# Kernel tuning notes

Measured on AMD Instinct MI355X. Metric: run time of the kernel, lower is better.

## Reference

```python
import jax, jax.numpy as jnp
import numpy as np

NV, NC = 4096, 16384        # n_vars, n_clauses
VL, CL = 8, 8               # vlabel_dim (ground_dim), clabel_dim
VE, CE = 128, 128           # vemb_dim, cemb_dim
ITERS = 4                   # max_iters
LN_EPS = 1e-5


def setup_inputs() -> dict:
    key = jax.random.key(0)
    ks = jax.random.split(key, 10)
    return {
        "vlabels": jax.random.normal(ks[0], (NV, VL), jnp.float32),
        "clabels": jax.random.normal(ks[1], (NC, CL), jnp.float32),
        "cmat_pos": jax.random.uniform(ks[2], (NC, NV), jnp.float32),
        "cmat_neg": jax.random.uniform(ks[3], (NC, NV), jnp.float32),
        "W_V_pos": jax.random.normal(ks[4], (VL + VE, CE), jnp.float32),
        "W_V_neg": jax.random.normal(ks[5], (VL + VE, CE), jnp.float32),
        "B_V": jax.random.normal(ks[6], (CE,), jnp.float32),
        "W_C_pos": jax.random.normal(ks[7], (CL + CE, VE), jnp.float32),
        "W_C_neg": jax.random.normal(ks[8], (CL + CE, VE), jnp.float32),
        "B_C": jax.random.normal(ks[9], (VE,), jnp.float32),
        "ln_gamma": jnp.ones((VE,), jnp.float32),
        "ln_beta": jnp.zeros((VE,), jnp.float32),
    }


def _layernorm(x, gamma, beta):
    mu = jnp.mean(x, axis=-1, keepdims=True)
    var = jnp.var(x, axis=-1, keepdims=True)
    return (x - mu) * jax.lax.rsqrt(var + LN_EPS) * gamma + beta


def reference(vlabels, clabels, cmat_pos, cmat_neg,
              W_V_pos, W_V_neg, B_V, W_C_pos, W_C_neg, B_C,
              ln_gamma, ln_beta):
    n_vars = vlabels.shape[0]
    vmat_pos = cmat_pos.T  # [NV, NC]
    vmat_neg = cmat_neg.T
    vembs0 = jnp.zeros((n_vars, VE), vlabels.dtype)

    def step(vembs, _):
        vs = jnp.concatenate([vlabels, vembs], axis=1)          # [NV, VL+VE]
        pv = vs @ W_V_pos                                       # [NV, CE]
        nv = vs @ W_V_neg
        cembs = jax.nn.relu(cmat_pos @ pv + cmat_neg @ nv + B_V)  # [NC, CE]
        cs = jnp.concatenate([clabels, cembs], axis=1)          # [NC, CL+CE]
        pc = cs @ W_C_pos                                       # [NC, VE]
        nc = cs @ W_C_neg
        v = jax.nn.relu(vmat_pos @ pc + vmat_neg @ nc + B_C)    # [NV, VE]
        v = _layernorm(v, ln_gamma, ln_beta)
        return v, None

    vembs, _ = jax.lax.scan(step, vembs0, None, length=ITERS)
    return vembs
```

## Files before the change

kernel.cpp:

```cpp
#include <hip/hip_runtime.h>

#define NVV 4096
#define NCC 16384
#define AS1 __attribute__((address_space(1)))
#define AS3 __attribute__((address_space(3)))

typedef __attribute__((ext_vector_type(8))) short short8;
typedef __attribute__((ext_vector_type(4))) short short4v;
typedef __attribute__((ext_vector_type(4))) float f32x4;

__device__ __forceinline__ short f2bf(float f) {
  union { float f; unsigned u; } v; v.f = f;
  unsigned r = v.u + 0x7fffu + ((v.u >> 16) & 1u);
  return (short)(r >> 16);
}

template<typename AT>
__device__ __forceinline__ short8 load8v(const AT* p) {
  if constexpr (sizeof(AT) == 2) {
    return *(const short8*)p;
  } else {
    const f32x4* q = (const f32x4*)p;
    f32x4 a = q[0], b = q[1];
    short8 o;
#pragma unroll
    for (int j = 0; j < 4; ++j) { o[j] = f2bf(a[j]); o[j + 4] = f2bf(b[j]); }
    return o;
  }
}

__global__ __launch_bounds__(256) void k_conv(const float* __restrict__ src,
                                              short* __restrict__ dst, int n8) {
  int i = blockIdx.x * blockDim.x + threadIdx.x;
  const int stride = gridDim.x * blockDim.x;
  for (; i < n8; i += stride) {
    const f32x4* q = (const f32x4*)(src + (size_t)i * 8);
    f32x4 a = q[0], b = q[1];
    short8 o;
#pragma unroll
    for (int j = 0; j < 4; ++j) { o[j] = f2bf(a[j]); o[j + 4] = f2bf(b[j]); }
    *(short8*)(dst + (size_t)i * 8) = o;
  }
}

__global__ __launch_bounds__(256) void k_convT(const float* __restrict__ src,
                                               short* __restrict__ dstN,
                                               short* __restrict__ dstT,
                                               int R, int C) {
  __shared__ short t[64][66];
  const int r0 = blockIdx.y * 64, c0 = blockIdx.x * 64;
  const int tr = threadIdx.x >> 2;
  const int q  = (threadIdx.x & 3) << 4;
  const float* s = src + (size_t)(r0 + tr) * C + c0 + q;
  const f32x4 v0 = *(const f32x4*)(s);
  const f32x4 v1 = *(const f32x4*)(s + 4);
  const f32x4 v2 = *(const f32x4*)(s + 8);
  const f32x4 v3 = *(const f32x4*)(s + 12);
  short8 a, b;
#pragma unroll
  for (int j = 0; j < 4; ++j) {
    a[j] = f2bf(v0[j]); a[4 + j] = f2bf(v1[j]);
    b[j] = f2bf(v2[j]); b[4 + j] = f2bf(v3[j]);
  }
  short* dn = dstN + (size_t)(r0 + tr) * C + c0 + q;
  *(short8*)dn = a;
  *(short8*)(dn + 8) = b;
#pragma unroll
  for (int j = 0; j < 8; ++j) { t[tr][q + j] = a[j]; t[tr][q + 8 + j] = b[j]; }
  __syncthreads();
  short8 oa, ob;
#pragma unroll
  for (int j = 0; j < 8; ++j) { oa[j] = t[q + j][tr]; ob[j] = t[q + 8 + j][tr]; }
  short* dt = dstT + (size_t)(c0 + tr) * R + r0 + q;
  *(short8*)dt = oa;
  *(short8*)(dt + 8) = ob;
}

template<int SRC, int NROW>
__global__ __launch_bounds__(128) void k_mlp(
    const float* __restrict__ labels, const float* __restrict__ embs,
    const float* __restrict__ bias,
    const float* __restrict__ Wp, const float* __restrict__ Wn,
    short* __restrict__ Tp, short* __restrict__ Tn, int Nrows, int KS) {
  __shared__ float xs[NROW][129];
  const int n = threadIdx.x;
  const int m0 = blockIdx.x * NROW;
  if (SRC == 1) {
#pragma unroll
    for (int r = 0; r < NROW; ++r)
      xs[r][n] = embs[(size_t)(m0 + r) * 128 + n];
    __syncthreads();
  } else if (SRC == 2) {
#pragma unroll
    for (int r = 0; r < NROW; ++r) {
      const size_t m = m0 + r;
      float v = bias[n];
      for (int ks = 0; ks < KS; ++ks)
        v += embs[((size_t)ks * NCC + m) * 128 + n];
      xs[r][n] = fmaxf(v, 0.f);
    }
    __syncthreads();
  }
  float ap[NROW] = {}, an[NROW] = {};
  const int JMAX = (SRC == 0) ? 8 : 136;
  for (int j = 0; j < JMAX; ++j) {
    const float wp = Wp[j * 128 + n], wn = Wn[j * 128 + n];
#pragma unroll
    for (int r = 0; r < NROW; ++r) {
      float x;
      if (j < 8) x = labels[(size_t)(m0 + r) * 8 + j];
      else       x = xs[r][j - 8];
      ap[r] = fmaf(x, wp, ap[r]);
      an[r] = fmaf(x, wn, an[r]);
    }
  }
  short8 vp0, vn0, vp1, vn1;
#pragma unroll
  for (int r = 0; r < 8; ++r) {
    vp0[r] = f2bf(ap[r]); vn0[r] = f2bf(an[r]);
    vp1[r] = f2bf(ap[8 + r]); vn1[r] = f2bf(an[8 + r]);
  }
  *(short8*)(Tp + (size_t)n * Nrows + m0) = vp0;
  *(short8*)(Tp + (size_t)n * Nrows + m0 + 8) = vp1;
  *(short8*)(Tn + (size_t)n * Nrows + m0) = vn0;
  *(short8*)(Tn + (size_t)n * Nrows + m0 + 8) = vn1;
}

template<int LSK>
__global__ __launch_bounds__(256, 2) void k_gemm8(
    const short* __restrict__ Ap, const short* __restrict__ An,
    const short* __restrict__ Bp, const short* __restrict__ Bn,
    float* __restrict__ C, int M, int lda, int ldb, int Klen) {
  __shared__ __align__(16) short sb[2][16384];
  const int tid = threadIdx.x;
  const int w = tid >> 6, l = tid & 63, lr = l & 15, lh = l >> 4;
  const int wr = w >> 1, wc = w & 1;
  const int id = blockIdx.x;
  const int zw = id & ((1 << LSK) - 1);
  const int m0 = (id >> LSK) * 128;
  const int Koff = zw * Klen;
  const int T = Klen >> 5;

  const int srow = (w << 4) + (l >> 2);
  const int scol = ((l & 3) ^ (srow & 3)) << 3;
  const short* gAp = Ap + (size_t)(m0 + srow) * lda + Koff + scol;
  const short* gAn = An + (size_t)(m0 + srow) * lda + Koff + scol;
  const short* gBp = Bp + (size_t)srow * ldb + Koff + scol;
  const short* gBn = Bn + (size_t)srow * ldb + Koff + scol;

  f32x4 acc[4][4] = {};

  auto stage = [&](int kstep, int buf) {
    const int k0 = kstep << 5;
    short* db = &sb[buf][0];
#pragma unroll
    for (int i = 0; i < 2; ++i) {
      const size_t ra = (size_t)(i * 64) * lda + k0;
      const size_t rb = (size_t)(i * 64) * ldb + k0;
      const int d = (i * 256 + w * 64) * 8;
      __builtin_amdgcn_global_load_lds((const AS1 void*)(gAp + ra),
                                       (AS3 void*)(db + d), 16, 0, 0);
      __builtin_amdgcn_global_load_lds((const AS1 void*)(gAn + ra),
                                       (AS3 void*)(db + 4096 + d), 16, 0, 0);
      __builtin_amdgcn_global_load_lds((const AS1 void*)(gBp + rb),
                                       (AS3 void*)(db + 8192 + d), 16, 0, 0);
      __builtin_amdgcn_global_load_lds((const AS1 void*)(gBn + rb),
                                       (AS3 void*)(db + 12288 + d), 16, 0, 0);
    }
  };

  stage(0, 0);
  asm volatile("s_waitcnt vmcnt(0)" ::: "memory");
  __builtin_amdgcn_s_barrier();
  asm volatile("" ::: "memory");

  for (int t = 0; t < T; ++t) {
    stage((t + 1 < T) ? t + 1 : 0, (t + 1) & 1);
    const short* bp = &sb[t & 1][0];
    short8 a[2][4], b[2][4];
#pragma unroll
    for (int mi = 0; mi < 4; ++mi) {
      const int row = (wr << 6) + (mi << 4) + lr;
      const int ad = (row << 5) + ((lh ^ (row & 3)) << 3);
      a[0][mi] = *(const short8*)&bp[ad];
      a[1][mi] = *(const short8*)&bp[4096 + ad];
    }
#pragma unroll
    for (int nj = 0; nj < 4; ++nj) {
      const int n = (wc << 6) + (nj << 4) + lr;
      const int bd = (n << 5) + ((lh ^ (n & 3)) << 3);
      b[0][nj] = *(const short8*)&bp[8192 + bd];
      b[1][nj] = *(const short8*)&bp[12288 + bd];
    }
#pragma unroll
    for (int mat = 0; mat < 2; ++mat)
#pragma unroll
      for (int mi = 0; mi < 4; ++mi)
#pragma unroll
        for (int nj = 0; nj < 4; ++nj)
          acc[mi][nj] = __builtin_amdgcn_mfma_f32_16x16x32_bf16(
              a[mat][mi], b[mat][nj], acc[mi][nj], 0, 0, 0);
    asm volatile("s_waitcnt vmcnt(0)" ::: "memory");
    __builtin_amdgcn_s_barrier();
    asm volatile("" ::: "memory");
  }

#pragma unroll
  for (int mi = 0; mi < 4; ++mi)
#pragma unroll
    for (int nj = 0; nj < 4; ++nj) {
      const int col = (wc << 6) + (nj << 4) + lr;
#pragma unroll
      for (int r = 0; r < 4; ++r) {
        const int m = m0 + (wr << 6) + (mi << 4) + (lh << 2) + r;
        C[((size_t)zw * M + m) * 128 + col] = acc[mi][nj][r];
      }
    }
}

template<typename AT, bool TRANSA, int EPI>
__global__ __launch_bounds__(256) void k_gemm(
    const AT* __restrict__ Ap, const AT* __restrict__ An,
    const short* __restrict__ Bp, const short* __restrict__ Bn,
    const float* __restrict__ bias, float* __restrict__ C,
    int M, int lda, int ldb, int Klen) {
  __shared__ __align__(16) short sA[2][32 * 64];
  __shared__ __align__(16) short sB[2][64 * 64];
  const int tid = threadIdx.x;
  const int w = tid >> 6, l = tid & 63, lr = l & 15, lh = l >> 4;
  const int m0 = blockIdx.x * 32, n0 = blockIdx.y * 64;
  const int Koff = blockIdx.z * Klen;
  f32x4 acc0 = {0.f, 0.f, 0.f, 0.f}, acc1 = {0.f, 0.f, 0.f, 0.f};

  for (int step = 0; step < (Klen >> 6); ++step) {
    const int k0 = Koff + (step << 6);
    __syncthreads();
    if (!TRANSA) {
      const int m = tid >> 3, kc = tid & 7;
      const size_t ga = (size_t)(m0 + m) * lda + k0 + (kc << 3);
      const int ad = (m << 6) + ((kc ^ (m & 7)) << 3);
      *(short8*)&sA[0][ad] = load8v(Ap + ga);
      *(short8*)&sA[1][ad] = load8v(An + ga);
    } else {
      const int r = tid >> 2, c8 = (tid & 3) << 3;
      const size_t ga = (size_t)(k0 + r) * lda + m0 + c8;
      short8 vp = load8v(Ap + ga), vn = load8v(An + ga);
#pragma unroll
      for (int j = 0; j < 8; ++j) {
        const int m = c8 + j;
        const int ad = (m << 6) + ((((r >> 3)) ^ (m & 7)) << 3) + (r & 7);
        sA[0][ad] = vp[j];
        sA[1][ad] = vn[j];
      }
    }
#pragma unroll
    for (int i = 0; i < 2; ++i) {
      const int c = (i << 8) + tid;
      const int n = c >> 3, kc = c & 7;
      const size_t gb = (size_t)(n0 + n) * ldb + k0 + (kc << 3);
      const int ad = (n << 6) + ((kc ^ (n & 7)) << 3);
      *(short8*)&sB[0][ad] = *(const short8*)(Bp + gb);
      *(short8*)&sB[1][ad] = *(const short8*)(Bn + gb);
    }
    __syncthreads();
#pragma unroll
    for (int kh = 0; kh < 2; ++kh) {
      const int kc = (kh << 2) + lh;
      const int bn_ = (w << 4) + lr;
      short8 bpv = *(short8*)&sB[0][(bn_ << 6) + ((kc ^ (bn_ & 7)) << 3)];
      short8 bnv = *(short8*)&sB[1][(bn_ << 6) + ((kc ^ (bn_ & 7)) << 3)];
      short8 a0p = *(short8*)&sA[0][(lr << 6) + ((kc ^ (lr & 7)) << 3)];
      short8 a0n = *(short8*)&sA[1][(lr << 6) + ((kc ^ (lr & 7)) << 3)];
      const int m1 = 16 + lr;
      short8 a1p = *(short8*)&sA[0][(m1 << 6) + ((kc ^ (m1 & 7)) << 3)];
      short8 a1n = *(short8*)&sA[1][(m1 << 6) + ((kc ^ (m1 & 7)) << 3)];
      acc0 = __builtin_amdgcn_mfma_f32_16x16x32_bf16(a0p, bpv, acc0, 0, 0, 0);
      acc0 = __builtin_amdgcn_mfma_f32_16x16x32_bf16(a0n, bnv, acc0, 0, 0, 0);
      acc1 = __builtin_amdgcn_mfma_f32_16x16x32_bf16(a1p, bpv, acc1, 0, 0, 0);
      acc1 = __builtin_amdgcn_mfma_f32_16x16x32_bf16(a1n, bnv, acc1, 0, 0, 0);
    }
  }
  const int n = n0 + (w << 4) + lr;
#pragma unroll
  for (int mf = 0; mf < 2; ++mf) {
    f32x4 a = mf ? acc1 : acc0;
#pragma unroll
    for (int r = 0; r < 4; ++r) {
      const int m = m0 + (mf << 4) + (lh << 2) + r;
      float c = a[r];
      if (EPI == 0) {
        c += bias[n];
        c = fmaxf(c, 0.f);
        C[(size_t)m * 128 + n] = c;
      } else {
        C[((size_t)blockIdx.z * M + m) * 128 + n] = c;
      }
    }
  }
}

template<int KS>
__global__ __launch_bounds__(256) void k_reduce_ln(
    const float* __restrict__ part, const float* __restrict__ bias,
    const float* __restrict__ gamma, const float* __restrict__ beta,
    float* __restrict__ out) {
  const int w = threadIdx.x >> 6, l = threadIdx.x & 63;
  const int m = blockIdx.x * 4 + w;
  const int n0 = l << 1;
  float x0 = bias[n0], x1 = bias[n0 + 1];
#pragma unroll
  for (int ks = 0; ks < KS; ++ks) {
    const size_t o = ((size_t)ks * NVV + m) * 128 + n0;
    x0 += part[o];
    x1 += part[o + 1];
  }
  x0 = fmaxf(x0, 0.f);
  x1 = fmaxf(x1, 0.f);
  float s = x0 + x1, q = x0 * x0 + x1 * x1;
#pragma unroll
  for (int off = 32; off; off >>= 1) {
    s += __shfl_xor(s, off);
    q += __shfl_xor(q, off);
  }
  const float mu = s * (1.f / 128.f);
  const float var = q * (1.f / 128.f) - mu * mu;
  const float inv = 1.f / sqrtf(var + 1e-5f);
  out[(size_t)m * 128 + n0]     = (x0 - mu) * inv * gamma[n0] + beta[n0];
  out[(size_t)m * 128 + n0 + 1] = (x1 - mu) * inv * gamma[n0 + 1] + beta[n0 + 1];
}

extern "C" void kernel_launch(void* const* d_in, const int* in_sizes, int n_in,
                              void* d_out, int out_size, void* d_ws, size_t ws_size,
                              hipStream_t stream) {
  const float* vlabels  = (const float*)d_in[0];
  const float* clabels  = (const float*)d_in[1];
  const float* cmat_pos = (const float*)d_in[2];
  const float* cmat_neg = (const float*)d_in[3];
  const float* Wvp = (const float*)d_in[4];
  const float* Wvn = (const float*)d_in[5];
  const float* Bv  = (const float*)d_in[6];
  const float* Wcp = (const float*)d_in[7];
  const float* Wcn = (const float*)d_in[8];
  const float* Bc  = (const float*)d_in[9];
  const float* gam = (const float*)d_in[10];
  const float* bet = (const float*)d_in[11];
  float* out = (float*)d_out;

  char* base = (char*)d_ws;
  const size_t SZ_vT = (size_t)128 * NVV * 2;
  const size_t SZ_cT = (size_t)128 * NCC * 2;
  const size_t SZ_cm = (size_t)NCC * NVV * 2;
  const size_t SZ_p8 = (size_t)NCC * 128 * 4;

  size_t o = 0;
  auto al = [&](size_t b) { size_t p = o; o += (b + 255) & ~(size_t)255; return p; };

  short* pvT  = (short*)(base + al(SZ_vT));
  short* nvT  = (short*)(base + al(SZ_vT));
  short* pcT  = (short*)(base + al(SZ_cT));
  short* ncT  = (short*)(base + al(SZ_cT));
  float* scr  = (float*)(base + al(4 * SZ_p8));
  short* cmPb = (short*)(base + al(SZ_cm));
  short* cmNb = (short*)(base + al(SZ_cm));
  short* cmTP = (short*)(base + al(SZ_cm));
  short* cmTN = (short*)(base + al(SZ_cm));
  const size_t needF = o;

  if (ws_size >= needF) {
    k_convT<<<dim3(NVV / 64, NCC / 64), 256, 0, stream>>>(cmat_pos, cmPb, cmTP, NCC, NVV);
    k_convT<<<dim3(NVV / 64, NCC / 64), 256, 0, stream>>>(cmat_neg, cmNb, cmTN, NCC, NVV);

    for (int it = 0; it < 4; ++it) {
      if (it == 0)
        k_mlp<0, 16><<<NVV / 16, 128, 0, stream>>>(vlabels, nullptr, nullptr, Wvp, Wvn, pvT, nvT, NVV, 0);
      else
        k_mlp<1, 16><<<NVV / 16, 128, 0, stream>>>(vlabels, out, nullptr, Wvp, Wvn, pvT, nvT, NVV, 0);

      k_gemm8<2><<<512, 256, 0, stream>>>(
          cmPb, cmNb, pvT, nvT, scr, NCC, NVV, NVV, NVV / 4);
      k_mlp<2, 16><<<NCC / 16, 128, 0, stream>>>(clabels, scr, Bv, Wcp, Wcn, pcT, ncT, NCC, 4);

      k_gemm8<4><<<512, 256, 0, stream>>>(
          cmTP, cmTN, pcT, ncT, scr, NVV, NCC, NCC, NCC / 16);
      k_reduce_ln<16><<<NVV / 4, 256, 0, stream>>>(scr, Bc, gam, bet, out);
    }
    return;
  }

  o = 0;
  pvT = (short*)(base + al(SZ_vT));
  nvT = (short*)(base + al(SZ_vT));
  pcT = (short*)(base + al(SZ_cT));
  ncT = (short*)(base + al(SZ_cT));
  float* part = (float*)(base + al(2 * SZ_p8));
  float* cemb = (float*)(base + al(SZ_p8));
  cmPb = (short*)(base + al(SZ_cm));
  cmNb = (short*)(base + al(SZ_cm));
  const size_t needN = o;
  const bool big = ws_size >= needN;

  if (big) {
    k_conv<<<4096, 256, 0, stream>>>(cmat_pos, cmPb, NCC * NVV / 8);
    k_conv<<<4096, 256, 0, stream>>>(cmat_neg, cmNb, NCC * NVV / 8);
  }

  for (int it = 0; it < 4; ++it) {
    if (it == 0)
      k_mlp<0, 16><<<NVV / 16, 128, 0, stream>>>(vlabels, nullptr, nullptr, Wvp, Wvn, pvT, nvT, NVV, 0);
    else
      k_mlp<1, 16><<<NVV / 16, 128, 0, stream>>>(vlabels, out, nullptr, Wvp, Wvn, pvT, nvT, NVV, 0);

    if (big) {
      k_gemm<short, false, 0><<<dim3(NCC / 32, 2, 1), 256, 0, stream>>>(
          cmPb, cmNb, pvT, nvT, Bv, cemb, NCC, NVV, NVV, NVV);
      k_mlp<1, 16><<<NCC / 16, 128, 0, stream>>>(clabels, cemb, nullptr, Wcp, Wcn, pcT, ncT, NCC, 0);
      k_gemm<short, true, 1><<<dim3(NVV / 32, 2, 4), 256, 0, stream>>>(
          cmPb, cmNb, pcT, ncT, nullptr, part, NVV, NVV, NCC, NVV);
      k_reduce_ln<4><<<NVV / 4, 256, 0, stream>>>(part, Bc, gam, bet, out);
    } else {
      k_gemm<float, false, 0><<<dim3(NCC / 32, 2, 1), 256, 0, stream>>>(
          cmat_pos, cmat_neg, pvT, nvT, Bv, cemb, NCC, NVV, NVV, NVV);
      k_mlp<1, 16><<<NCC / 16, 128, 0, stream>>>(clabels, cemb, nullptr, Wcp, Wcn, pcT, ncT, NCC, 0);
      k_gemm<float, true, 1><<<dim3(NVV / 32, 2, 4), 256, 0, stream>>>(
          cmat_pos, cmat_neg, pcT, ncT, nullptr, part, NVV, NVV, NCC, NVV);
      k_reduce_ln<4><<<NVV / 4, 256, 0, stream>>>(part, Bc, gam, bet, out);
    }
  }
}
```

Before: 1.558 ms.

## Pre-pack clause matrices into tile-contiguous swizzled blocks for GEMM staging

Replaces the separate convert/transpose kernels with a single packing kernel that writes both cmat_pos/cmat_neg and their transposes in bf16 as contiguous 128x32 k-step tiles with the LDS swizzle baked in. The MLP kernels emit their outputs in the same packed B layout, and a new GEMM kernel stages each k-step with fully contiguous 16-byte loads instead of strided row reads. The aim is cheaper, more coalesced global-to-LDS traffic and one fused pre-pass over both matrices. The trade-offs are a more involved pack kernel with heavy LDS use and the MLP row block growing to 32 rows, which raises register pressure.

```diff
diff --git a/kernel.cpp b/kernel.cpp
--- a/kernel.cpp
+++ b/kernel.cpp
@@ -29,6 +29,203 @@
   }
 }
 
+
+__global__ __launch_bounds__(256, 2) void k_pack(
+    const float* __restrict__ srcP, const float* __restrict__ srcN,
+    short* __restrict__ packN, short* __restrict__ packT, int R, int C) {
+  __shared__ short ts[8 * 4240];
+  const int t = threadIdx.x;
+  const int r0 = blockIdx.y * 128, c0 = blockIdx.x * 256;
+  const int nksN = C >> 5, nksT = R >> 5;
+  const int rowl = t >> 3;
+  const int ks8 = t & 7;
+
+  for (int mat = 0; mat < 2; ++mat) {
+    const float* src = mat ? srcN : srcP;
+#pragma unroll
+    for (int pass = 0; pass < 4; ++pass) {
+      const int row = pass * 32 + rowl;
+      const float* s = src + (size_t)(r0 + row) * C + c0 + ks8 * 32;
+      short b[32];
+#pragma unroll
+      for (int i = 0; i < 8; ++i) {
+        f32x4 q = *(const f32x4*)(s + i * 4);
+#pragma unroll
+        for (int j = 0; j < 4; ++j) b[i * 4 + j] = f2bf(q[j]);
+      }
+      short* cb = packN + ((size_t)blockIdx.y * nksN + (c0 >> 5) + ks8) * 8192
+                  + mat * 4096 + row * 32;
+#pragma unroll
+      for (int kp = 0; kp < 4; ++kp) {
+        short8 o;
+#pragma unroll
+        for (int j = 0; j < 8; ++j) o[j] = b[kp * 8 + j];
+        *(short8*)(cb + ((kp ^ (row & 3)) << 3)) = o;
+      }
+#pragma unroll
+      for (int j = 0; j < 32; ++j) {
+        const int vloc = ks8 * 32 + j;
+        const int s8 = ((row >> 6) << 2) + (vloc >> 6);
+        ts[s8 * 4240 + (row & 63) * 66 + (vloc & 63)] = b[j];
+      }
+    }
+    __syncthreads();
+    {
+      const int vloc = t;
+      const int vtile = (blockIdx.x << 1) + (vloc >> 7);
+      const int vrow = vloc & 127;
+      short* vb = packT + (size_t)vtile * nksT * 8192;
+#pragma unroll
+      for (int kp16 = 0; kp16 < 16; ++kp16) {
+        const int cbase = kp16 * 8;
+        short8 o;
+#pragma unroll
+        for (int i = 0; i < 8; ++i) {
+          const int c = cbase + i;
+          const int s8 = ((c >> 6) << 2) + (vloc >> 6);
+          o[i] = ts[s8 * 4240 + (c & 63) * 66 + (vloc & 63)];
+        }
+        const int kstep = (r0 >> 5) + (kp16 >> 2);
+        const int kp = kp16 & 3;
+        *(short8*)(vb + (size_t)kstep * 8192 + mat * 4096 + vrow * 32
+                   + ((kp ^ (vrow & 3)) << 3)) = o;
+      }
+    }
+    __syncthreads();
+  }
+}
+
+template<int SRC>
+__global__ __launch_bounds__(128) void k_mlp_pk(
+    const float* __restrict__ labels, const float* __restrict__ embs,
+    const float* __restrict__ bias,
+    const float* __restrict__ Wp, const float* __restrict__ Wn,
+    short* __restrict__ Bpack, int Nrows, int KS) {
+  __shared__ float xs[32][129];
+  const int n = threadIdx.x;
+  const int m0 = blockIdx.x * 32;
+  if (SRC == 1) {
+#pragma unroll
+    for (int r = 0; r < 32; ++r)
+      xs[r][n] = embs[(size_t)(m0 + r) * 128 + n];
+    __syncthreads();
+  } else if (SRC == 2) {
+#pragma unroll
+    for (int r = 0; r < 32; ++r) {
+      const size_t m = m0 + r;
+      float v = bias[n];
+      for (int ks = 0; ks < KS; ++ks)
+        v += embs[((size_t)ks * NCC + m) * 128 + n];
+      xs[r][n] = fmaxf(v, 0.f);
+    }
+    __syncthreads();
+  }
+  float ap[32] = {}, an[32] = {};
+  const int JMAX = (SRC == 0) ? 8 : 136;
+  for (int j = 0; j < JMAX; ++j) {
+    const float wp = Wp[j * 128 + n], wn = Wn[j * 128 + n];
+#pragma unroll
+    for (int r = 0; r < 32; ++r) {
+      const float x = (j < 8) ? labels[(size_t)(m0 + r) * 8 + j] : xs[r][j - 8];
+      ap[r] = fmaf(x, wp, ap[r]);
+      an[r] = fmaf(x, wn, an[r]);
+    }
+  }
+  short* cb = Bpack + (size_t)(m0 >> 5) * 8192 + n * 32;
+#pragma unroll
+  for (int kp = 0; kp < 4; ++kp) {
+    short8 op, on;
+#pragma unroll
+    for (int j = 0; j < 8; ++j) { op[j] = f2bf(ap[kp * 8 + j]); on[j] = f2bf(an[kp * 8 + j]); }
+    *(short8*)(cb + ((kp ^ (n & 3)) << 3)) = op;
+    *(short8*)(cb + 4096 + ((kp ^ (n & 3)) << 3)) = on;
+  }
+}
+
+template<int EPI, int LSK>
+__global__ __launch_bounds__(256, 2) void k_gemm9(
+    const short* __restrict__ Apack, const short* __restrict__ Bpack,
+    const float* __restrict__ bias, float* __restrict__ C,
+    int M, int nks, int T) {
+  __shared__ __align__(16) short sb[2][16384];
+  const int tid = threadIdx.x;
+  const int w = tid >> 6, l = tid & 63, lr = l & 15, lh = l >> 4;
+  const int wr = w >> 1, wc = w & 1;
+  const int id = blockIdx.x;
+  const int zw = id & ((1 << LSK) - 1);
+  const int mtile = id >> LSK;
+  const short* aB = Apack + ((size_t)mtile * nks + (size_t)zw * T) * 8192;
+  const short* bB = Bpack + (size_t)zw * T * 8192;
+  const int soff = w * 2048 + l * 8;
+
+  auto stage = [&](int t, int buf) {
+    const short* a = aB + (size_t)t * 8192;
+    const short* b = bB + (size_t)t * 8192;
+    short* d = &sb[buf][0];
+#pragma unroll
+    for (int i = 0; i < 4; ++i) {
+      const int o = soff + i * 512;
+      __builtin_amdgcn_global_load_lds((const AS1 void*)(a + o),
+                                       (AS3 void*)(d + o), 16, 0, 0);
+      __builtin_amdgcn_global_load_lds((const AS1 void*)(b + o),
+                                       (AS3 void*)(d + 8192 + o), 16, 0, 0);
+    }
+  };
+
+  f32x4 acc[4][4] = {};
+  stage(0, 0);
+  asm volatile("s_waitcnt vmcnt(0)" ::: "memory");
+  __builtin_amdgcn_s_barrier();
+  asm volatile("" ::: "memory");
+
+  for (int t = 0; t < T; ++t) {
+    stage((t + 1 < T) ? t + 1 : 0, (t + 1) & 1);
+    const short* bp = &sb[t & 1][0];
+    short8 a[2][4], b[2][4];
+#pragma unroll
+    for (int mi = 0; mi < 4; ++mi) {
+      const int row = (wr << 6) + (mi << 4) + lr;
+      const int ad = (row << 5) + ((lh ^ (row & 3)) << 3);
+      a[0][mi] = *(const short8*)&bp[ad];
+      a[1][mi] = *(const short8*)&bp[4096 + ad];
+    }
+#pragma unroll
+    for (int nj = 0; nj < 4; ++nj) {
+      const int nn = (wc << 6) + (nj << 4) + lr;
+      const int bd = (nn << 5) + ((lh ^ (nn & 3)) << 3);
+      b[0][nj] = *(const short8*)&bp[8192 + bd];
+      b[1][nj] = *(const short8*)&bp[12288 + bd];
+    }
+#pragma unroll
+    for (int mat = 0; mat < 2; ++mat)
+#pragma unroll
+      for (int mi = 0; mi < 4; ++mi)
+#pragma unroll
+        for (int nj = 0; nj < 4; ++nj)
+          acc[mi][nj] = __builtin_amdgcn_mfma_f32_16x16x32_bf16(
+              a[mat][mi], b[mat][nj], acc[mi][nj], 0, 0, 0);
+    asm volatile("s_waitcnt vmcnt(0)" ::: "memory");
+    __builtin_amdgcn_s_barrier();
+    asm volatile("" ::: "memory");
+  }
+
+#pragma unroll
+  for (int mi = 0; mi < 4; ++mi)
+#pragma unroll
+    for (int nj = 0; nj < 4; ++nj) {
+      const int col = (wc << 6) + (nj << 4) + lr;
+#pragma unroll
+      for (int r = 0; r < 4; ++r) {
+        const int m = (mtile << 7) + (wr << 6) + (mi << 4) + (lh << 2) + r;
+        if (EPI == 0) {
+          C[(size_t)m * 128 + col] = fmaxf(acc[mi][nj][r] + bias[col], 0.f);
+        } else {
+          C[((size_t)zw * M + m) * 128 + col] = acc[mi][nj][r];
+        }
+      }
+    }
+}
+
 __global__ __launch_bounds__(256) void k_conv(const float* __restrict__ src,
                                               short* __restrict__ dst, int n8) {
   int i = blockIdx.x * blockDim.x + threadIdx.x;
@@ -41,39 +238,6 @@
     for (int j = 0; j < 4; ++j) { o[j] = f2bf(a[j]); o[j + 4] = f2bf(b[j]); }
     *(short8*)(dst + (size_t)i * 8) = o;
   }
-}
-
-__global__ __launch_bounds__(256) void k_convT(const float* __restrict__ src,
-                                               short* __restrict__ dstN,
-                                               short* __restrict__ dstT,
-                                               int R, int C) {
-  __shared__ short t[64][66];
-  const int r0 = blockIdx.y * 64, c0 = blockIdx.x * 64;
-  const int tr = threadIdx.x >> 2;
-  const int q  = (threadIdx.x & 3) << 4;
-  const float* s = src + (size_t)(r0 + tr) * C + c0 + q;
-  const f32x4 v0 = *(const f32x4*)(s);
-  const f32x4 v1 = *(const f32x4*)(s + 4);
-  const f32x4 v2 = *(const f32x4*)(s + 8);
-  const f32x4 v3 = *(const f32x4*)(s + 12);
-  short8 a, b;
-#pragma unroll
-  for (int j = 0; j < 4; ++j) {
-    a[j] = f2bf(v0[j]); a[4 + j] = f2bf(v1[j]);
-    b[j] = f2bf(v2[j]); b[4 + j] = f2bf(v3[j]);
-  }
-  short* dn = dstN + (size_t)(r0 + tr) * C + c0 + q;
-  *(short8*)dn = a;
-  *(short8*)(dn + 8) = b;
-#pragma unroll
-  for (int j = 0; j < 8; ++j) { t[tr][q + j] = a[j]; t[tr][q + 8 + j] = b[j]; }
-  __syncthreads();
-  short8 oa, ob;
-#pragma unroll
-  for (int j = 0; j < 8; ++j) { oa[j] = t[q + j][tr]; ob[j] = t[q + 8 + j][tr]; }
-  short* dt = dstT + (size_t)(c0 + tr) * R + r0 + q;
-  *(short8*)dt = oa;
-  *(short8*)(dt + 8) = ob;
 }
 
 template<int SRC, int NROW>
@@ -90,16 +254,6 @@
     for (int r = 0; r < NROW; ++r)
       xs[r][n] = embs[(size_t)(m0 + r) * 128 + n];
     __syncthreads();
-  } else if (SRC == 2) {
-#pragma unroll
-    for (int r = 0; r < NROW; ++r) {
-      const size_t m = m0 + r;
-      float v = bias[n];
-      for (int ks = 0; ks < KS; ++ks)
-        v += embs[((size_t)ks * NCC + m) * 128 + n];
-      xs[r][n] = fmaxf(v, 0.f);
-    }
-    __syncthreads();
   }
   float ap[NROW] = {}, an[NROW] = {};
   const int JMAX = (SRC == 0) ? 8 : 136;
@@ -107,9 +261,7 @@
     const float wp = Wp[j * 128 + n], wn = Wn[j * 128 + n];
 #pragma unroll
     for (int r = 0; r < NROW; ++r) {
-      float x;
-      if (j < 8) x = labels[(size_t)(m0 + r) * 8 + j];
-      else       x = xs[r][j - 8];
+      const float x = (j < 8) ? labels[(size_t)(m0 + r) * 8 + j] : xs[r][j - 8];
       ap[r] = fmaf(x, wp, ap[r]);
       an[r] = fmaf(x, wn, an[r]);
     }
@@ -124,98 +276,6 @@
   *(short8*)(Tp + (size_t)n * Nrows + m0 + 8) = vp1;
   *(short8*)(Tn + (size_t)n * Nrows + m0) = vn0;
   *(short8*)(Tn + (size_t)n * Nrows + m0 + 8) = vn1;
-}
-
-template<int LSK>
-__global__ __launch_bounds__(256, 2) void k_gemm8(
-    const short* __restrict__ Ap, const short* __restrict__ An,
-    const short* __restrict__ Bp, const short* __restrict__ Bn,
-    float* __restrict__ C, int M, int lda, int ldb, int Klen) {
-  __shared__ __align__(16) short sb[2][16384];
-  const int tid = threadIdx.x;
-  const int w = tid >> 6, l = tid & 63, lr = l & 15, lh = l >> 4;
-  const int wr = w >> 1, wc = w & 1;
-  const int id = blockIdx.x;
-  const int zw = id & ((1 << LSK) - 1);
-  const int m0 = (id >> LSK) * 128;
-  const int Koff = zw * Klen;
-  const int T = Klen >> 5;
-
-  const int srow = (w << 4) + (l >> 2);
-  const int scol = ((l & 3) ^ (srow & 3)) << 3;
-  const short* gAp = Ap + (size_t)(m0 + srow) * lda + Koff + scol;
-  const short* gAn = An + (size_t)(m0 + srow) * lda + Koff + scol;
-  const short* gBp = Bp + (size_t)srow * ldb + Koff + scol;
-  const short* gBn = Bn + (size_t)srow * ldb + Koff + scol;
-
-  f32x4 acc[4][4] = {};
-
-  auto stage = [&](int kstep, int buf) {
-    const int k0 = kstep << 5;
-    short* db = &sb[buf][0];
-#pragma unroll
-    for (int i = 0; i < 2; ++i) {
-      const size_t ra = (size_t)(i * 64) * lda + k0;
-      const size_t rb = (size_t)(i * 64) * ldb + k0;
-      const int d = (i * 256 + w * 64) * 8;
-      __builtin_amdgcn_global_load_lds((const AS1 void*)(gAp + ra),
-                                       (AS3 void*)(db + d), 16, 0, 0);
-      __builtin_amdgcn_global_load_lds((const AS1 void*)(gAn + ra),
-                                       (AS3 void*)(db + 4096 + d), 16, 0, 0);
-      __builtin_amdgcn_global_load_lds((const AS1 void*)(gBp + rb),
-                                       (AS3 void*)(db + 8192 + d), 16, 0, 0);
-      __builtin_amdgcn_global_load_lds((const AS1 void*)(gBn + rb),
-                                       (AS3 void*)(db + 12288 + d), 16, 0, 0);
-    }
-  };
-
-  stage(0, 0);
-  asm volatile("s_waitcnt vmcnt(0)" ::: "memory");
-  __builtin_amdgcn_s_barrier();
-  asm volatile("" ::: "memory");
-
-  for (int t = 0; t < T; ++t) {
-    stage((t + 1 < T) ? t + 1 : 0, (t + 1) & 1);
-    const short* bp = &sb[t & 1][0];
-    short8 a[2][4], b[2][4];
-#pragma unroll
-    for (int mi = 0; mi < 4; ++mi) {
-      const int row = (wr << 6) + (mi << 4) + lr;
-      const int ad = (row << 5) + ((lh ^ (row & 3)) << 3);
-      a[0][mi] = *(const short8*)&bp[ad];
-      a[1][mi] = *(const short8*)&bp[4096 + ad];
-    }
-#pragma unroll
-    for (int nj = 0; nj < 4; ++nj) {
-      const int n = (wc << 6) + (nj << 4) + lr;
-      const int bd = (n << 5) + ((lh ^ (n & 3)) << 3);
-      b[0][nj] = *(const short8*)&bp[8192 + bd];
-      b[1][nj] = *(const short8*)&bp[12288 + bd];
-    }
-#pragma unroll
-    for (int mat = 0; mat < 2; ++mat)
-#pragma unroll
-      for (int mi = 0; mi < 4; ++mi)
-#pragma unroll
-        for (int nj = 0; nj < 4; ++nj)
-          acc[mi][nj] = __builtin_amdgcn_mfma_f32_16x16x32_bf16(
-              a[mat][mi], b[mat][nj], acc[mi][nj], 0, 0, 0);
-    asm volatile("s_waitcnt vmcnt(0)" ::: "memory");
-    __builtin_amdgcn_s_barrier();
-    asm volatile("" ::: "memory");
-  }
-
-#pragma unroll
-  for (int mi = 0; mi < 4; ++mi)
-#pragma unroll
-    for (int nj = 0; nj < 4; ++nj) {
-      const int col = (wc << 6) + (nj << 4) + lr;
-#pragma unroll
-      for (int r = 0; r < 4; ++r) {
-        const int m = m0 + (wr << 6) + (mi << 4) + (lh << 2) + r;
-        C[((size_t)zw * M + m) * 128 + col] = acc[mi][nj][r];
-      }
-    }
 }
 
 template<typename AT, bool TRANSA, int EPI>
@@ -347,55 +407,52 @@
   float* out = (float*)d_out;
 
   char* base = (char*)d_ws;
-  const size_t SZ_vT = (size_t)128 * NVV * 2;
-  const size_t SZ_cT = (size_t)128 * NCC * 2;
-  const size_t SZ_cm = (size_t)NCC * NVV * 2;
-  const size_t SZ_p8 = (size_t)NCC * 128 * 4;
+  const size_t SZ_vpk = (size_t)(NVV / 32) * 16384;
+  const size_t SZ_cpk = (size_t)(NCC / 32) * 16384;
+  const size_t SZ_p8  = (size_t)NCC * 128 * 4;
+  const size_t SZ_pk  = (size_t)NCC * NVV * 2;
+  const size_t SZ_cm  = SZ_pk;
 
   size_t o = 0;
   auto al = [&](size_t b) { size_t p = o; o += (b + 255) & ~(size_t)255; return p; };
 
-  short* pvT  = (short*)(base + al(SZ_vT));
-  short* nvT  = (short*)(base + al(SZ_vT));
-  short* pcT  = (short*)(base + al(SZ_cT));
-  short* ncT  = (short*)(base + al(SZ_cT));
-  float* scr  = (float*)(base + al(4 * SZ_p8));
+  short* vpack  = (short*)(base + al(SZ_vpk));
+  short* cpack  = (short*)(base + al(SZ_cpk));
+  float* scr    = (float*)(base + al(4 * SZ_p8));
+  short* packA1 = (short*)(base + al(2 * SZ_pk));
+  short* packA2 = (short*)(base + al(2 * SZ_pk));
+  const size_t needF = o;
+
+  if (ws_size >= needF) {
+    k_pack<<<dim3(NVV / 256, NCC / 128), 256, 0, stream>>>(
+        cmat_pos, cmat_neg, packA1, packA2, NCC, NVV);
+
+    for (int it = 0; it < 4; ++it) {
+      if (it == 0)
+        k_mlp_pk<0><<<NVV / 32, 128, 0, stream>>>(vlabels, nullptr, nullptr, Wvp, Wvn, vpack, NVV, 0);
+      else
+        k_mlp_pk<1><<<NVV / 32, 128, 0, stream>>>(vlabels, out, nullptr, Wvp, Wvn, vpack, NVV, 0);
+
+      k_gemm9<1, 2><<<512, 256, 0, stream>>>(
+          packA1, vpack, nullptr, scr, NCC, NVV / 32, NVV / 32 / 4);
+      k_mlp_pk<2><<<NCC / 32, 128, 0, stream>>>(clabels, scr, Bv, Wcp, Wcn, cpack, NCC, 4);
+
+      k_gemm9<1, 4><<<512, 256, 0, stream>>>(
+          packA2, cpack, nullptr, scr, NVV, NCC / 32, NCC / 32 / 16);
+      k_reduce_ln<16><<<NVV / 4, 256, 0, stream>>>(scr, Bc, gam, bet, out);
+    }
+    return;
+  }
+
+  o = 0;
+  short* pvT = (short*)(base + al((size_t)128 * NVV * 2));
+  short* nvT = (short*)(base + al((size_t)128 * NVV * 2));
+  short* pcT = (short*)(base + al((size_t)128 * NCC * 2));
+  short* ncT = (short*)(base + al((size_t)128 * NCC * 2));
+  float* part = (float*)(base + al(2 * SZ_p8));
+  float* cemb = (float*)(base + al(SZ_p8));
   short* cmPb = (short*)(base + al(SZ_cm));
   short* cmNb = (short*)(base + al(SZ_cm));
-  short* cmTP = (short*)(base + al(SZ_cm));
-  short* cmTN = (short*)(base + al(SZ_cm));
-  const size_t needF = o;
-
-  if (ws_size >= needF) {
-    k_convT<<<dim3(NVV / 64, NCC / 64), 256, 0, stream>>>(cmat_pos, cmPb, cmTP, NCC, NVV);
-    k_convT<<<dim3(NVV / 64, NCC / 64), 256, 0, stream>>>(cmat_neg, cmNb, cmTN, NCC, NVV);
-
-    for (int it = 0; it < 4; ++it) {
-      if (it == 0)
-        k_mlp<0, 16><<<NVV / 16, 128, 0, stream>>>(vlabels, nullptr, nullptr, Wvp, Wvn, pvT, nvT, NVV, 0);
-      else
-        k_mlp<1, 16><<<NVV / 16, 128, 0, stream>>>(vlabels, out, nullptr, Wvp, Wvn, pvT, nvT, NVV, 0);
-
-      k_gemm8<2><<<512, 256, 0, stream>>>(
-          cmPb, cmNb, pvT, nvT, scr, NCC, NVV, NVV, NVV / 4);
-      k_mlp<2, 16><<<NCC / 16, 128, 0, stream>>>(clabels, scr, Bv, Wcp, Wcn, pcT, ncT, NCC, 4);
-
-      k_gemm8<4><<<512, 256, 0, stream>>>(
-          cmTP, cmTN, pcT, ncT, scr, NVV, NCC, NCC, NCC / 16);
-      k_reduce_ln<16><<<NVV / 4, 256, 0, stream>>>(scr, Bc, gam, bet, out);
-    }
-    return;
-  }
-
-  o = 0;
-  pvT = (short*)(base + al(SZ_vT));
-  nvT = (short*)(base + al(SZ_vT));
-  pcT = (short*)(base + al(SZ_cT));
-  ncT = (short*)(base + al(SZ_cT));
-  float* part = (float*)(base + al(2 * SZ_p8));
-  float* cemb = (float*)(base + al(SZ_p8));
-  cmPb = (short*)(base + al(SZ_cm));
-  cmNb = (short*)(base + al(SZ_cm));
   const size_t needN = o;
   const bool big = ws_size >= needN;
 
```

New measurement: 2.118 ms. +36.0%, slower.
